# Performance work log

Measured on AMD Instinct MI355X. Metric: run time of the kernel, lower is better.

The kernel has to match this reference:

```python
import jax, jax.numpy as jnp
import numpy as np

EPS = 1e-8

def l2norm(x, axis=-1):
    norm = jnp.sqrt(jnp.sum(x * x, axis=axis, keepdims=True)) + EPS
    return x / norm


def setup_inputs() -> dict:
    key = jax.random.key(0)
    ks = jax.random.split(key, 16)
    B, N, IMG_DIM, EMBED = 256, 36, 2048, 1024
    DK = EMBED // 8  # 128
    H3 = 3 * EMBED
    r_wl = float(np.sqrt(6.0) / np.sqrt(IMG_DIM + EMBED))
    r_k = float(np.sqrt(6.0) / np.sqrt(EMBED + DK))
    r_v = float(np.sqrt(6.0) / np.sqrt(EMBED + EMBED))
    sg = 1.0 / np.sqrt(EMBED)  # torch GRU default init range
    return {
        "images": jax.random.normal(ks[0], (B, N, IMG_DIM), jnp.float32),
        "oimages": jax.random.normal(ks[1], (B, EMBED), jnp.float32),
        "wl_w": jax.random.uniform(ks[2], (EMBED, IMG_DIM), jnp.float32, -r_wl, r_wl),
        "wl_b": jnp.zeros((EMBED,), jnp.float32),
        "wk_w": jax.random.uniform(ks[3], (DK, EMBED), jnp.float32, -r_k, r_k),
        "wk_b": jnp.zeros((DK,), jnp.float32),
        "wq_w": jax.random.uniform(ks[4], (DK, EMBED), jnp.float32, -r_k, r_k),
        "wq_b": jnp.zeros((DK,), jnp.float32),
        "wv_w": jax.random.uniform(ks[5], (EMBED, EMBED), jnp.float32, -r_v, r_v),
        "wv_b": jnp.zeros((EMBED,), jnp.float32),
        "gru_wih": jax.random.uniform(ks[6], (H3, EMBED), jnp.float32, -sg, sg),
        "gru_whh": jax.random.uniform(ks[7], (H3, EMBED), jnp.float32, -sg, sg),
        "gru_bih": jax.random.uniform(ks[8], (H3,), jnp.float32, -sg, sg),
        "gru_bhh": jax.random.uniform(ks[9], (H3,), jnp.float32, -sg, sg),
    }


def gru_last_hidden(x, wih, whh, bih, bhh):
    # Single-layer batch_first GRU (torch gate order r, z, n); returns final hidden h_N.
    B, N, H = x.shape[0], x.shape[1], whh.shape[1]
    gi = jnp.einsum('bnd,gd->bng', x, wih) + bih  # (B, N, 3H), input gates precomputed

    def step(h, gi_t):
        gh = h @ whh.T + bhh
        ir, iz, inn = jnp.split(gi_t, 3, axis=-1)
        hr, hz, hn = jnp.split(gh, 3, axis=-1)
        r = jax.nn.sigmoid(ir + hr)
        z = jax.nn.sigmoid(iz + hz)
        n = jnp.tanh(inn + r * hn)
        h_new = (1.0 - z) * n + z * h
        return h_new, None

    h0 = jnp.zeros((B, H), x.dtype)
    hN, _ = jax.lax.scan(step, h0, jnp.swapaxes(gi, 0, 1))
    return hN


def reference(images, oimages, wl_w, wl_b, wk_w, wk_b, wq_w, wq_b, wv_w, wv_b,
              gru_wih, gru_whh, gru_bih, gru_bhh):
    dk = wk_w.shape[0]
    f = jnp.einsum('bni,ei->bne', images, wl_w) + wl_b      # (B, N, E)
    f = l2norm(f, axis=-1)
    f = f + oimages[:, None, :]                              # broadcast add

    k = jnp.einsum('bne,de->bnd', f, wk_w) + wk_b            # (B, N, dk)
    q = jnp.einsum('bne,de->bnd', f, wq_w) + wq_b            # (B, N, dk)
    scores = jnp.einsum('bid,bjd->bij', k, q) / jnp.sqrt(jnp.asarray(dk, f.dtype))
    w_mn = jax.nn.softmax(scores, axis=2)                    # (B, N, N)
    v = jnp.einsum('bne,de->bnd', f, wv_w) + wv_b            # (B, N, E)
    # Original torch code: (w_mn[b,i,j] * v[b,i,d]).sum(j) -> v scaled by row-sums
    # of the softmax (== 1). Expressed faithfully without the BxNxNxE intermediate:
    attn = jnp.sum(w_mn, axis=2)[..., None] * v              # == v
    f = attn + f

    hN = gru_last_hidden(f, gru_wih, gru_whh, gru_bih, gru_bhh)  # out[:, N-1, :]
    return l2norm(hN, axis=-1)
```

## Files before the change

kernel.cpp:

```cpp
#include <hip/hip_runtime.h>
#include <hip/hip_bf16.h>

#define DEVI __device__ __forceinline__

typedef short bf16x8 __attribute__((ext_vector_type(8)));
typedef float f32x4 __attribute__((ext_vector_type(4)));


DEVI unsigned short f2b(float f) {
    union { float f; unsigned u; } x; x.f = f;
    unsigned r = x.u + 0x7fffu + ((x.u >> 16) & 1u);
    return (unsigned short)(r >> 16);
}

DEVI float b2f(unsigned short u) {
    union { unsigned u; float f; } x; x.u = ((unsigned)u) << 16; return x.f;
}

DEVI void gld_lds16(const void* g, void* l) {
    __builtin_amdgcn_global_load_lds(
        (const __attribute__((address_space(1))) void*)g,
        (__attribute__((address_space(3))) void*)l, 16, 0, 0);
}


__global__ __launch_bounds__(256) void cvt_f32_bf16(
    const float* __restrict__ src, unsigned short* __restrict__ dst, int n4)
{
    int stride = gridDim.x * 256;
    for (int i = blockIdx.x * 256 + threadIdx.x; i < n4; i += stride) {
        float4 v = reinterpret_cast<const float4*>(src)[i];
        ushort4 o;
        o.x = f2b(v.x); o.y = f2b(v.y); o.z = f2b(v.z); o.w = f2b(v.w);
        reinterpret_cast<ushort4*>(dst)[i] = o;
    }
}


template<int EPI>
__global__ __launch_bounds__(256) void gemm_bt(
    const unsigned short* __restrict__ A, const unsigned short* __restrict__ Bm,
    const float* __restrict__ bias, const float* resid,
    float* outF, unsigned short* outB,
    int Mn, int Nn, int K, int mtiles)
{
    __shared__ short lds[2][2][128 * 32];
    const int tid = threadIdx.x;
    const int lane = tid & 63, w = tid >> 6;
    const int bid = blockIdx.x;
    const int mt = bid % mtiles, nt = bid / mtiles;
    const int m0 = mt * 128, n0 = nt * 128;
    const int fr = lane & 15, kg = lane >> 4;
    const int wr = (w >> 1) * 64, wc = (w & 1) * 64;

    auto stage = [&](int buf, int k0) {
#pragma unroll
        for (int rnd = 0; rnd < 2; ++rnd) {
            int chunk = rnd * 256 + w * 64;
            int slot = chunk + lane;
            int row = slot >> 2, ks = slot & 3;
            gld_lds16(A + (size_t)(m0 + row) * K + k0 + ks * 8,
                      (void*)&lds[buf][0][chunk * 8]);
        }
#pragma unroll
        for (int rnd = 0; rnd < 2; ++rnd) {
            int chunk = rnd * 256 + w * 64;
            int slot = chunk + lane;
            int row = slot >> 2, ks = slot & 3;
            gld_lds16(Bm + (size_t)(n0 + row) * K + k0 + ks * 8,
                      (void*)&lds[buf][1][chunk * 8]);
        }
    };

    f32x4 acc[4][4] = {};

    stage(0, 0);
    __syncthreads();
    const int nk = K >> 5;
    for (int kt = 0; kt < nk; ++kt) {
        int buf = kt & 1;
        if (kt + 1 < nk) stage(buf ^ 1, (kt + 1) * 32);
        const short* As = lds[buf][0];
        const short* Bs = lds[buf][1];
        bf16x8 af[4], bfv[4];
#pragma unroll
        for (int m = 0; m < 4; ++m)
            af[m] = *(const bf16x8*)&As[(wr + m * 16 + fr) * 32 + kg * 8];
#pragma unroll
        for (int n = 0; n < 4; ++n)
            bfv[n] = *(const bf16x8*)&Bs[(wc + n * 16 + fr) * 32 + kg * 8];
#pragma unroll
        for (int m = 0; m < 4; ++m)
#pragma unroll
            for (int n = 0; n < 4; ++n)
                acc[m][n] = __builtin_amdgcn_mfma_f32_16x16x32_bf16(
                    af[m], bfv[n], acc[m][n], 0, 0, 0);
        __syncthreads();
    }

#pragma unroll
    for (int n = 0; n < 4; ++n) {
        int col = n0 + wc + n * 16 + fr;
        float bc = bias[col];
#pragma unroll
        for (int m = 0; m < 4; ++m) {
            f32x4 v = acc[m][n];
#pragma unroll
            for (int i = 0; i < 4; ++i) {
                int row = m0 + wr + m * 16 + kg * 4 + i;
                size_t idx = (size_t)row * Nn + col;
                float val = v[i] + bc;
                if (EPI == 0) {
                    outF[idx] = val;
                } else if (EPI == 1) {
                    outB[idx] = f2b(val);
                } else {
                    val += resid[idx];
                    outB[idx] = f2b(val);
                }
            }
        }
    }
}


__global__ __launch_bounds__(256) void l2norm_add(
    const float* fin, const float* __restrict__ oimg,
    float* foutF, unsigned short* __restrict__ foutB)
{
    int row = blockIdx.x;
    int b = row / 36;
    float4 v = reinterpret_cast<const float4*>(fin + (size_t)row * 1024)[threadIdx.x];
    float s = v.x * v.x + v.y * v.y + v.z * v.z + v.w * v.w;
#pragma unroll
    for (int o = 32; o; o >>= 1) s += __shfl_down(s, o, 64);
    __shared__ float ws4[4];
    int lane = threadIdx.x & 63, w = threadIdx.x >> 6;
    if (lane == 0) ws4[w] = s;
    __syncthreads();
    float tot = ws4[0] + ws4[1] + ws4[2] + ws4[3];
    float inv = 1.0f / (sqrtf(tot) + 1e-8f);
    float4 o4 = reinterpret_cast<const float4*>(oimg + (size_t)b * 1024)[threadIdx.x];
    float4 y;
    y.x = v.x * inv + o4.x; y.y = v.y * inv + o4.y;
    y.z = v.z * inv + o4.z; y.w = v.w * inv + o4.w;
    reinterpret_cast<float4*>(foutF + (size_t)row * 1024)[threadIdx.x] = y;
    ushort4 yb; yb.x = f2b(y.x); yb.y = f2b(y.y); yb.z = f2b(y.z); yb.w = f2b(y.w);
    reinterpret_cast<ushort4*>(foutB + (size_t)row * 1024)[threadIdx.x] = yb;
}


__global__ __launch_bounds__(256) void gru_step(
    const unsigned short* __restrict__ hb, const float* __restrict__ hf,
    const unsigned short* __restrict__ whh, const unsigned short* __restrict__ gi,
    const float* __restrict__ bhh,
    float* __restrict__ hfo, unsigned short* __restrict__ hbo, int t)
{
    __shared__ short lds[2][64 * 32 + 48 * 32];
    const int tid = threadIdx.x, lane = tid & 63, w = tid >> 6;
    const int bid = blockIdx.x;
    const int b0 = (bid & 3) * 64;
    const int e0 = (bid >> 2) * 16;
    const int fr = lane & 15, kg = lane >> 4;

    auto stage = [&](int buf, int k0) {
        {
            int chunk = w * 64, slot = chunk + lane;
            int row = slot >> 2, ks = slot & 3;
            gld_lds16(hb + (size_t)(b0 + row) * 1024 + k0 + ks * 8,
                      (void*)&lds[buf][chunk * 8]);
        }
        if (w < 3) {
            int chunk = w * 64, slot = chunk + lane;
            int j = slot >> 2, ks = slot & 3;
            int g = j >> 4, c = j & 15;
            gld_lds16(whh + (size_t)(g * 1024 + e0 + c) * 1024 + k0 + ks * 8,
                      (void*)&lds[buf][64 * 32 + chunk * 8]);
        }
    };

    f32x4 acc[3] = {};
    stage(0, 0);
    __syncthreads();
    for (int kt = 0; kt < 32; ++kt) {
        int buf = kt & 1;
        if (kt < 31) stage(buf ^ 1, (kt + 1) * 32);
        const short* Hs = lds[buf];
        const short* Ws = lds[buf] + 64 * 32;
        bf16x8 a = *(const bf16x8*)&Hs[(w * 16 + fr) * 32 + kg * 8];
#pragma unroll
        for (int g = 0; g < 3; ++g) {
            bf16x8 bb = *(const bf16x8*)&Ws[(g * 16 + fr) * 32 + kg * 8];
            acc[g] = __builtin_amdgcn_mfma_f32_16x16x32_bf16(a, bb, acc[g], 0, 0, 0);
        }
        __syncthreads();
    }

    const int e = e0 + fr;
    const float bhr = bhh[e], bhz = bhh[1024 + e], bhn = bhh[2048 + e];
#pragma unroll
    for (int i = 0; i < 4; ++i) {
        int b = b0 + w * 16 + kg * 4 + i;
        const unsigned short* gir = gi + ((size_t)b * 36 + t) * 3072;
        float ir = b2f(gir[e]), iz = b2f(gir[1024 + e]), inn = b2f(gir[2048 + e]);
        float ghr = acc[0][i] + bhr;
        float ghz = acc[1][i] + bhz;
        float ghn = acc[2][i] + bhn;
        float r = 1.f / (1.f + __expf(-(ir + ghr)));
        float z = 1.f / (1.f + __expf(-(iz + ghz)));
        float n = tanhf(inn + r * ghn);
        float hold = hf[(size_t)b * 1024 + e];
        float hnew = (1.f - z) * n + z * hold;
        hfo[(size_t)b * 1024 + e] = hnew;
        hbo[(size_t)b * 1024 + e] = f2b(hnew);
    }
}

__global__ __launch_bounds__(256) void zero_h(float* hf0, unsigned short* hb0) {
    int i = blockIdx.x * 256 + threadIdx.x;
    hf0[i] = 0.f;
    hb0[i] = 0;
}

__global__ __launch_bounds__(256) void final_norm(
    const float* __restrict__ hf, float* __restrict__ out)
{
    int row = blockIdx.x;
    float4 v = reinterpret_cast<const float4*>(hf + (size_t)row * 1024)[threadIdx.x];
    float s = v.x * v.x + v.y * v.y + v.z * v.z + v.w * v.w;
#pragma unroll
    for (int o = 32; o; o >>= 1) s += __shfl_down(s, o, 64);
    __shared__ float ws4[4];
    int lane = threadIdx.x & 63, w = threadIdx.x >> 6;
    if (lane == 0) ws4[w] = s;
    __syncthreads();
    float tot = ws4[0] + ws4[1] + ws4[2] + ws4[3];
    float inv = 1.0f / (sqrtf(tot) + 1e-8f);
    float4 y; y.x = v.x * inv; y.y = v.y * inv; y.z = v.z * inv; y.w = v.w * inv;
    reinterpret_cast<float4*>(out + (size_t)row * 1024)[threadIdx.x] = y;
}


extern "C" void kernel_launch(void* const* d_in, const int* in_sizes, int n_in,
                              void* d_out, int out_size, void* d_ws, size_t ws_size,
                              hipStream_t stream)
{
    constexpr int cB = 256, cN = 36, cIMG = 2048, cE = 1024, cH3 = 3072;
    constexpr int cM = cB * cN;

    const float* images  = (const float*)d_in[0];
    const float* oimages = (const float*)d_in[1];
    const float* wl_w    = (const float*)d_in[2];
    const float* wl_b    = (const float*)d_in[3];
    const float* wv_w    = (const float*)d_in[8];
    const float* wv_b    = (const float*)d_in[9];
    const float* wih     = (const float*)d_in[10];
    const float* whh     = (const float*)d_in[11];
    const float* bih     = (const float*)d_in[12];
    const float* bhh     = (const float*)d_in[13];

    char* ws = (char*)d_ws;
    size_t off = 0;
    auto alloc = [&](size_t bytes) -> char* {
        char* p = ws + off; off += (bytes + 255) & ~(size_t)255; return p;
    };
    unsigned short* imgB = (unsigned short*)alloc((size_t)cM * cIMG * 2);
    unsigned short* wlB  = (unsigned short*)alloc((size_t)cE * cIMG * 2);
    unsigned short* wvB  = (unsigned short*)alloc((size_t)cE * cE * 2);
    unsigned short* wihB = (unsigned short*)alloc((size_t)cH3 * cE * 2);
    unsigned short* whhB = (unsigned short*)alloc((size_t)cH3 * cE * 2);
    float*          fpre = (float*)alloc((size_t)cM * cE * 4);
    unsigned short* fB   = (unsigned short*)alloc((size_t)cM * cE * 2);
    unsigned short* f2B  = (unsigned short*)alloc((size_t)cM * cE * 2);
    unsigned short* giB  = (unsigned short*)alloc((size_t)cM * cH3 * 2);
    float*          hf0  = (float*)alloc((size_t)cB * cE * 4);
    float*          hf1  = (float*)alloc((size_t)cB * cE * 4);
    unsigned short* hb0  = (unsigned short*)alloc((size_t)cB * cE * 2);
    unsigned short* hb1  = (unsigned short*)alloc((size_t)cB * cE * 2);
    (void)ws_size;

    cvt_f32_bf16<<<2048, 256, 0, stream>>>(images, imgB, cM * cIMG / 4);
    cvt_f32_bf16<<<512, 256, 0, stream>>>(wl_w, wlB, cE * cIMG / 4);
    cvt_f32_bf16<<<256, 256, 0, stream>>>(wv_w, wvB, cE * cE / 4);
    cvt_f32_bf16<<<512, 256, 0, stream>>>(wih, wihB, cH3 * cE / 4);
    cvt_f32_bf16<<<512, 256, 0, stream>>>(whh, whhB, cH3 * cE / 4);

    gemm_bt<0><<<72 * 8, 256, 0, stream>>>(imgB, wlB, wl_b, nullptr,
                                           fpre, nullptr, cM, cE, cIMG, 72);
    l2norm_add<<<cM, 256, 0, stream>>>(fpre, oimages, fpre, fB);

    gemm_bt<2><<<72 * 8, 256, 0, stream>>>(fB, wvB, wv_b, fpre,
                                           nullptr, f2B, cM, cE, cE, 72);
    gemm_bt<1><<<72 * 24, 256, 0, stream>>>(f2B, wihB, bih, nullptr,
                                            nullptr, giB, cM, cH3, cE, 72);

    zero_h<<<1024, 256, 0, stream>>>(hf0, hb0);
    float* hfp[2] = { hf0, hf1 };
    unsigned short* hbp[2] = { hb0, hb1 };
    for (int t = 0; t < 36; ++t) {
        gru_step<<<256, 256, 0, stream>>>(hbp[t & 1], hfp[t & 1], whhB, giB, bhh,
                                          hfp[(t + 1) & 1], hbp[(t + 1) & 1], t);
    }
    final_norm<<<cB, 256, 0, stream>>>(hf0, (float*)d_out);
}
```

Before: 680.0 us.

## Fuse GRU timesteps into one persistent cooperative kernel with LDS-resident weights

Replaces the 36 per-timestep GRU kernel launches with one cooperative persistent kernel. Each block keeps its 48x1024 slice of W_hh resident in swizzled LDS, holds the hidden state in registers, and uses a custom atomic grid barrier between steps. The input-gate GEMM epilogue now writes gi in time-major layout so per-step reads are contiguous. This removes launch overhead and repeated reloading of W_hh and the fp32 hidden state, but adds a spin barrier with a guard timeout and needs all 256 blocks to be co-resident.

```diff
diff --git a/kernel.cpp b/kernel.cpp
--- a/kernel.cpp
+++ b/kernel.cpp
@@ -5,6 +5,8 @@
 
 typedef short bf16x8 __attribute__((ext_vector_type(8)));
 typedef float f32x4 __attribute__((ext_vector_type(4)));
+
+#define NBLK 256
 
 
 DEVI unsigned short f2b(float f) {
@@ -108,15 +110,16 @@
 #pragma unroll
             for (int i = 0; i < 4; ++i) {
                 int row = m0 + wr + m * 16 + kg * 4 + i;
-                size_t idx = (size_t)row * Nn + col;
                 float val = v[i] + bc;
                 if (EPI == 0) {
-                    outF[idx] = val;
-                } else if (EPI == 1) {
+                    outF[(size_t)row * Nn + col] = val;
+                } else if (EPI == 2) {
+                    size_t idx = (size_t)row * Nn + col;
+                    val += resid[idx];
                     outB[idx] = f2b(val);
                 } else {
-                    val += resid[idx];
-                    outB[idx] = f2b(val);
+                    int b = row / 36, t = row - b * 36;
+                    outB[(size_t)(t * 256 + b) * Nn + col] = f2b(val);
                 }
             }
         }
@@ -150,76 +153,132 @@
 }
 
 
-__global__ __launch_bounds__(256) void gru_step(
-    const unsigned short* __restrict__ hb, const float* __restrict__ hf,
-    const unsigned short* __restrict__ whh, const unsigned short* __restrict__ gi,
+DEVI void pgrid_sync(unsigned* bar, unsigned gen) {
+    __syncthreads();
+    if (blockIdx.x == 0) {
+        int b = threadIdx.x;
+        if (b > 0) {
+            int guard = 0;
+            while (__hip_atomic_load(&bar[b * 16], __ATOMIC_ACQUIRE,
+                                     __HIP_MEMORY_SCOPE_AGENT) < gen) {
+                __builtin_amdgcn_s_sleep(1);
+                if (++guard > (1 << 22)) break;
+            }
+        }
+        __syncthreads();
+        if (threadIdx.x == 0)
+            __hip_atomic_store(&bar[NBLK * 16], gen, __ATOMIC_RELEASE,
+                               __HIP_MEMORY_SCOPE_AGENT);
+    } else {
+        if (threadIdx.x == 0) {
+            __hip_atomic_store(&bar[blockIdx.x * 16], gen, __ATOMIC_RELEASE,
+                               __HIP_MEMORY_SCOPE_AGENT);
+            int guard = 0;
+            while (__hip_atomic_load(&bar[NBLK * 16], __ATOMIC_ACQUIRE,
+                                     __HIP_MEMORY_SCOPE_AGENT) < gen) {
+                __builtin_amdgcn_s_sleep(1);
+                if (++guard > (1 << 22)) break;
+            }
+        }
+        __syncthreads();
+    }
+}
+
+
+__global__ __launch_bounds__(256, 1) void gru_persist(
+    const unsigned short* __restrict__ whhB,
+    const unsigned short* __restrict__ giB,
     const float* __restrict__ bhh,
-    float* __restrict__ hfo, unsigned short* __restrict__ hbo, int t)
-{
-    __shared__ short lds[2][64 * 32 + 48 * 32];
+    unsigned short* __restrict__ hA,
+    unsigned short* __restrict__ hBb,
+    float* __restrict__ hfin,
+    unsigned* __restrict__ bar)
+{
+    __shared__ short whs[48 * 1024];
     const int tid = threadIdx.x, lane = tid & 63, w = tid >> 6;
-    const int bid = blockIdx.x;
-    const int b0 = (bid & 3) * 64;
-    const int e0 = (bid >> 2) * 16;
+    const int wg = blockIdx.x;
+    const int b0 = (wg & 3) * 64;
+    const int e0 = (wg >> 2) * 16;
     const int fr = lane & 15, kg = lane >> 4;
-
-    auto stage = [&](int buf, int k0) {
-        {
-            int chunk = w * 64, slot = chunk + lane;
-            int row = slot >> 2, ks = slot & 3;
-            gld_lds16(hb + (size_t)(b0 + row) * 1024 + k0 + ks * 8,
-                      (void*)&lds[buf][chunk * 8]);
-        }
-        if (w < 3) {
-            int chunk = w * 64, slot = chunk + lane;
-            int j = slot >> 2, ks = slot & 3;
-            int g = j >> 4, c = j & 15;
-            gld_lds16(whh + (size_t)(g * 1024 + e0 + c) * 1024 + k0 + ks * 8,
-                      (void*)&lds[buf][64 * 32 + chunk * 8]);
-        }
-    };
-
-    f32x4 acc[3] = {};
-    stage(0, 0);
-    __syncthreads();
-    for (int kt = 0; kt < 32; ++kt) {
-        int buf = kt & 1;
-        if (kt < 31) stage(buf ^ 1, (kt + 1) * 32);
-        const short* Hs = lds[buf];
-        const short* Ws = lds[buf] + 64 * 32;
-        bf16x8 a = *(const bf16x8*)&Hs[(w * 16 + fr) * 32 + kg * 8];
-#pragma unroll
-        for (int g = 0; g < 3; ++g) {
-            bf16x8 bb = *(const bf16x8*)&Ws[(g * 16 + fr) * 32 + kg * 8];
-            acc[g] = __builtin_amdgcn_mfma_f32_16x16x32_bf16(a, bb, acc[g], 0, 0, 0);
-        }
-        __syncthreads();
-    }
+    const int sz = fr & 7;
+
+    for (int it = 0; it < 24; ++it) {
+        int slot = it * 256 + tid;
+        int j = slot >> 7, pc = slot & 127;
+        int gc = pc ^ (j & 7);
+        int grow = (j >> 4) * 1024 + e0 + (j & 15);
+        gld_lds16(whhB + (size_t)grow * 1024 + gc * 8, (void*)&whs[slot * 8]);
+    }
+    __syncthreads();
 
     const int e = e0 + fr;
     const float bhr = bhh[e], bhz = bhh[1024 + e], bhn = bhh[2048 + e];
-#pragma unroll
-    for (int i = 0; i < 4; ++i) {
-        int b = b0 + w * 16 + kg * 4 + i;
-        const unsigned short* gir = gi + ((size_t)b * 36 + t) * 3072;
-        float ir = b2f(gir[e]), iz = b2f(gir[1024 + e]), inn = b2f(gir[2048 + e]);
-        float ghr = acc[0][i] + bhr;
-        float ghz = acc[1][i] + bhz;
-        float ghn = acc[2][i] + bhn;
-        float r = 1.f / (1.f + __expf(-(ir + ghr)));
-        float z = 1.f / (1.f + __expf(-(iz + ghz)));
-        float n = tanhf(inn + r * ghn);
-        float hold = hf[(size_t)b * 1024 + e];
-        float hnew = (1.f - z) * n + z * hold;
-        hfo[(size_t)b * 1024 + e] = hnew;
-        hbo[(size_t)b * 1024 + e] = f2b(hnew);
-    }
-}
-
-__global__ __launch_bounds__(256) void zero_h(float* hf0, unsigned short* hb0) {
+    float hreg[4] = {0.f, 0.f, 0.f, 0.f};
+    int bb[4];
+#pragma unroll
+    for (int i = 0; i < 4; ++i) bb[i] = b0 + w * 16 + kg * 4 + i;
+    const int arow = b0 + w * 16 + fr;
+
+    unsigned short* hbuf[2] = { hA, hBb };
+
+    for (int t = 0; t < 36; ++t) {
+        const unsigned short* hc = hbuf[t & 1];
+        unsigned short* hn = hbuf[(t + 1) & 1];
+
+        const unsigned short* gbase = giB + (size_t)t * 256 * 3072 + e;
+        unsigned short giu[4][3];
+#pragma unroll
+        for (int i = 0; i < 4; ++i) {
+            const unsigned short* g = gbase + (size_t)bb[i] * 3072;
+            giu[i][0] = g[0]; giu[i][1] = g[1024]; giu[i][2] = g[2048];
+        }
+
+        const unsigned short* hrow = hc + (size_t)arow * 1024 + kg * 8;
+        bf16x8 av[32];
+#pragma unroll
+        for (int kt = 0; kt < 32; ++kt)
+            av[kt] = *(const bf16x8*)(hrow + kt * 32);
+
+        f32x4 a0 = {}, a1 = {}, a2 = {};
+#pragma unroll
+        for (int kt = 0; kt < 32; ++kt) {
+            const int c0 = kt * 4 + kg;
+            bf16x8 w0 = *(const bf16x8*)&whs[(0 * 16 + fr) * 1024 + ((c0 ^ sz) << 3)];
+            a0 = __builtin_amdgcn_mfma_f32_16x16x32_bf16(av[kt], w0, a0, 0, 0, 0);
+            bf16x8 w1 = *(const bf16x8*)&whs[(1 * 16 + fr) * 1024 + ((c0 ^ sz) << 3)];
+            a1 = __builtin_amdgcn_mfma_f32_16x16x32_bf16(av[kt], w1, a1, 0, 0, 0);
+            bf16x8 w2 = *(const bf16x8*)&whs[(2 * 16 + fr) * 1024 + ((c0 ^ sz) << 3)];
+            a2 = __builtin_amdgcn_mfma_f32_16x16x32_bf16(av[kt], w2, a2, 0, 0, 0);
+        }
+
+#pragma unroll
+        for (int i = 0; i < 4; ++i) {
+            float ir = b2f(giu[i][0]), iz = b2f(giu[i][1]), inn = b2f(giu[i][2]);
+            float r = 1.f / (1.f + __expf(-(ir + a0[i] + bhr)));
+            float z = 1.f / (1.f + __expf(-(iz + a1[i] + bhz)));
+            float n = tanhf(inn + r * (a2[i] + bhn));
+            hreg[i] = (1.f - z) * n + z * hreg[i];
+        }
+
+        if (t == 35) {
+#pragma unroll
+            for (int i = 0; i < 4; ++i)
+                hfin[(size_t)bb[i] * 1024 + e] = hreg[i];
+        } else {
+#pragma unroll
+            for (int i = 0; i < 4; ++i)
+                hn[(size_t)bb[i] * 1024 + e] = f2b(hreg[i]);
+            pgrid_sync(bar, (unsigned)(t + 1));
+        }
+    }
+}
+
+__global__ __launch_bounds__(256) void zero_state(
+    unsigned short* hb0, unsigned* bar)
+{
     int i = blockIdx.x * 256 + threadIdx.x;
-    hf0[i] = 0.f;
-    hb0[i] = 0;
+    if (i < 256 * 1024) hb0[i] = 0;
+    if (i < 8192) bar[i] = 0;
 }
 
 __global__ __launch_bounds__(256) void final_norm(
@@ -273,10 +332,10 @@
     unsigned short* fB   = (unsigned short*)alloc((size_t)cM * cE * 2);
     unsigned short* f2B  = (unsigned short*)alloc((size_t)cM * cE * 2);
     unsigned short* giB  = (unsigned short*)alloc((size_t)cM * cH3 * 2);
-    float*          hf0  = (float*)alloc((size_t)cB * cE * 4);
-    float*          hf1  = (float*)alloc((size_t)cB * cE * 4);
+    float*          hfin = (float*)alloc((size_t)cB * cE * 4);
     unsigned short* hb0  = (unsigned short*)alloc((size_t)cB * cE * 2);
     unsigned short* hb1  = (unsigned short*)alloc((size_t)cB * cE * 2);
+    unsigned*       bar  = (unsigned*)alloc(8192 * 4);
     (void)ws_size;
 
     cvt_f32_bf16<<<2048, 256, 0, stream>>>(images, imgB, cM * cIMG / 4);
@@ -291,15 +350,15 @@
 
     gemm_bt<2><<<72 * 8, 256, 0, stream>>>(fB, wvB, wv_b, fpre,
                                            nullptr, f2B, cM, cE, cE, 72);
-    gemm_bt<1><<<72 * 24, 256, 0, stream>>>(f2B, wihB, bih, nullptr,
+    gemm_bt<3><<<72 * 24, 256, 0, stream>>>(f2B, wihB, bih, nullptr,
                                             nullptr, giB, cM, cH3, cE, 72);
 
-    zero_h<<<1024, 256, 0, stream>>>(hf0, hb0);
-    float* hfp[2] = { hf0, hf1 };
-    unsigned short* hbp[2] = { hb0, hb1 };
-    for (int t = 0; t < 36; ++t) {
-        gru_step<<<256, 256, 0, stream>>>(hbp[t & 1], hfp[t & 1], whhB, giB, bhh,
-                                          hfp[(t + 1) & 1], hbp[(t + 1) & 1], t);
-    }
-    final_norm<<<cB, 256, 0, stream>>>(hf0, (float*)d_out);
-}
+    zero_state<<<1024, 256, 0, stream>>>(hb0, bar);
+
+    void* args[] = { (void*)&whhB, (void*)&giB, (void*)&bhh, (void*)&hb0,
+                     (void*)&hb1, (void*)&hfin, (void*)&bar };
+    hipLaunchCooperativeKernel((void*)gru_persist, dim3(NBLK), dim3(256),
+                               args, 0, stream);
+
+    final_norm<<<cB, 256, 0, stream>>>(hfin, (float*)d_out);
+}
```

After: 1.459 ms. +114.6%, slower.
